# Kernel optimization log

Hardware: AMD Instinct MI355X
Metric: run time of the kernel (lower is better)

Reference implementation:

```python
import jax, jax.numpy as jnp
import numpy as np
from jax import lax

B, H, W, C = 8, 128, 128, 256


def setup_inputs() -> dict:
    key = jax.random.key(0)
    k1, k2 = jax.random.split(key)
    x = jax.random.normal(k1, (B, H, W, C), dtype=jnp.float32)
    # small-magnitude kernel so predicted offsets stay moderate (like trained init)
    kernel = jax.random.normal(k2, (3, 3, C, 2 * C), dtype=jnp.float32) * 0.01
    bias = jnp.zeros((2 * C,), dtype=jnp.float32)
    return {"x": x, "kernel": kernel, "bias": bias}


def _deform_sample(x, kernel, bias):
    b, h, w, c = x.shape
    # offset prediction conv: (b,h,w,c) -> (b,h,w,2c), SAME padding, stride 1
    offsets = lax.conv_general_dilated(
        x, kernel, window_strides=(1, 1), padding="SAME",
        dimension_numbers=("NHWC", "HWIO", "NHWC")) + bias
    # faithful reshape scaffolding from the original keras layer
    # (b,h,w,2c) -> (b,2c,h,w) -> (b*c, h, w, 2)
    offs = jnp.transpose(offsets, (0, 3, 1, 2)).reshape(b * c, h, w, 2)
    # (b,h,w,c) -> (b*c, h, w)
    xb = jnp.transpose(x, (0, 3, 1, 2)).reshape(b * c, h, w)

    n = h * w
    offs = offs.reshape(b * c, n, 2)
    grid = jnp.stack(jnp.meshgrid(jnp.arange(h), jnp.arange(w), indexing="ij"), axis=-1)
    grid = grid.reshape(n, 2).astype(x.dtype)  # (n,2) absolute (i,j)
    coords = offs + grid  # (b*c, n, 2)

    # original clips coord0 by w-1 and coord1 by h-1 (h==w assumed)
    c0 = jnp.clip(coords[..., 0], 0.0, jnp.float32(w - 1))
    c1 = jnp.clip(coords[..., 1], 0.0, jnp.float32(h - 1))
    coords = jnp.stack([c0, c1], axis=-1)

    lt = jnp.floor(coords).astype(jnp.int32)  # (b*c, n, 2)
    rb = jnp.ceil(coords).astype(jnp.int32)

    bidx = jnp.arange(b * c)[:, None]  # (b*c, 1) broadcast over n
    vals_lt = xb[bidx, lt[..., 0], lt[..., 1]]
    vals_rb = xb[bidx, rb[..., 0], rb[..., 1]]
    vals_lb = xb[bidx, lt[..., 0], rb[..., 1]]
    vals_rt = xb[bidx, rb[..., 0], lt[..., 1]]

    frac = coords - lt.astype(coords.dtype)  # (b*c, n, 2)
    vals_t = vals_lt + (vals_rt - vals_lt) * frac[..., 0]
    vals_b = vals_lb + (vals_rb - vals_lb) * frac[..., 0]
    mapped = vals_t + (vals_b - vals_t) * frac[..., 1]  # (b*c, n)

    # (b*c, h*w) -> (b, c, h, w) -> (b, h, w, c)
    return jnp.transpose(mapped.reshape(b, c, h, w), (0, 2, 3, 1))


def reference(x, kernel, bias):
    return _deform_sample(x, kernel, bias)
```

## Files before the change

kernel.cpp:

```cpp
#include <hip/hip_runtime.h>
#include <hip/hip_bf16.h>

#define BATCH 8
#define HH 128
#define WW 128
#define CC 256
#define OCC 512

typedef __bf16 bf16x8 __attribute__((ext_vector_type(8)));
typedef unsigned int u32x4 __attribute__((ext_vector_type(4)));
typedef float f32x4 __attribute__((ext_vector_type(4)));

#define WT_OFF   0
#define ZROW_OFF 2359296
#define XTB_OFF  2424832
#define XBF_OFF  69533696

__global__ void prep_weights(const float* __restrict__ k, __bf16* __restrict__ wt) {
    const int n   = blockIdx.x & 511;
    const int tap = blockIdx.x >> 9;
    const int ic  = threadIdx.x;
    const int oc  = ((n & 255) << 1) | (n >> 8);
    wt[((size_t)(tap * OCC + n)) * CC + ic] = (__bf16)k[((size_t)(tap * CC + ic)) * OCC + oc];
}

__global__ void zero_fill(float* __restrict__ z) {
    z[blockIdx.x * 256 + threadIdx.x] = 0.0f;
}

__global__ __launch_bounds__(256)
void prep_x(const float* __restrict__ x, __bf16* __restrict__ xbf, __bf16* __restrict__ xtb) {
    __shared__ float tile[64][65];
    const int pt = blockIdx.x & 3;
    const int mt = (blockIdx.x >> 2) & 255;
    const int b  = blockIdx.x >> 10;
    const int m0 = mt * 64, p0 = pt * 64;
    const int tl = threadIdx.x & 63, tr = threadIdx.x >> 6;

    const float* xb = x + (size_t)b * (HH * WW * CC);
    __bf16* xbfb = xbf + (size_t)b * (HH * WW * CC);
#pragma unroll
    for (int rr = 0; rr < 16; ++rr) {
        const int m = rr * 4 + tr;
        const float v = xb[(size_t)(m0 + m) * CC + p0 + tl];
        tile[m][tl] = v;
        xbfb[(size_t)(m0 + m) * CC + p0 + tl] = (__bf16)v;
    }
    __syncthreads();
    __bf16* xtbb = xtb + (size_t)b * (CC * HH * WW);
#pragma unroll
    for (int rr = 0; rr < 16; ++rr) {
        const int p = rr * 4 + tr;
        xtbb[(size_t)(p0 + p) * (HH * WW) + m0 + tl] = (__bf16)tile[tl][p];
    }
}

__device__ __forceinline__ void gload16(const void* g, void* l) {
    __builtin_amdgcn_global_load_lds(
        (const __attribute__((address_space(1))) void*)g,
        (__attribute__((address_space(3))) void*)l, 16, 0, 0);
}

__device__ __forceinline__ void stage_chunk(const __bf16* __restrict__ srcrow, int h,
                                            __bf16* ldsbuf, int wid, int lane) {
    const int sub = lane >> 4;
    const int icb = (lane & 15) * 16;
#pragma unroll
    for (int t = 0; t < 8; ++t) {
        const int col = (wid * 8 + t) * 4 + sub;
        const int srcoff = col * 512 + h * 256 + (icb ^ ((col & 7) << 4));
        gload16((const char*)srcrow + srcoff, (char*)ldsbuf + (wid * 8 + t) * 1024);
    }
}

__global__ __launch_bounds__(256, 2)
void conv_offset_sample(const __bf16* __restrict__ xbf, const __bf16* __restrict__ xtb,
                        const __bf16* __restrict__ zrow, const __bf16* __restrict__ wt,
                        const float* __restrict__ bias, float* __restrict__ out) {
    __shared__ __bf16 lds_a[2][16384];

    const int orig = blockIdx.x;
    const int bi = (orig & 7) * 512 + (orig >> 3);
    const int nc = bi & 3;
    const int cr = (bi >> 2) & 127;
    const int b  = bi >> 9;

    const int tid  = threadIdx.x;
    const int lane = tid & 63;
    const int wid  = tid >> 6;
    const int l15  = lane & 15;
    const int lg   = lane >> 4;

    f32x4 acc[2][8] = {};

    {
        const int rg = cr - 1;
        const __bf16* srcrow = ((unsigned)rg < 128u) ? xbf + ((size_t)(b * 128 + rg) << 15) : zrow;
        stage_chunk(srcrow, 0, lds_a[0], wid, lane);
    }
    __syncthreads();

    int cur = 0;
#pragma unroll 1
    for (int idx = 0; idx < 6; ++idx) {
        if (idx < 5) {
            const int n2 = idx + 1;
            const int rg = cr + (n2 >> 1) - 1;
            const __bf16* srcrow = ((unsigned)rg < 128u) ? xbf + ((size_t)(b * 128 + rg) << 15) : zrow;
            stage_chunk(srcrow, n2 & 1, lds_a[cur ^ 1], wid, lane);
        }
        const int r = idx >> 1;
        const int h = idx & 1;
        const __bf16* Ab = lds_a[cur];
        const int colb = wid * 32;

#pragma unroll
        for (int dx = 0; dx < 3; ++dx) {
            const __bf16* wtap = wt + ((size_t)((r * 3 + dx) * OCC + nc * 128)) * CC + h * 128;
#pragma unroll
            for (int kk = 0; kk < 4; ++kk) {
                bf16x8 a[2];
#pragma unroll
                for (int mi = 0; mi < 2; ++mi) {
                    const int ca = colb + mi * 16 + l15 + dx - 1;
                    const unsigned msk = ((unsigned)ca < 128u) ? 0xFFFFFFFFu : 0u;
                    const int ad = (((ca & 127) << 8) + ((kk * 32 + lg * 8) << 1)) ^ ((ca & 7) << 4);
                    u32x4 uv = *(const u32x4*)((const char*)Ab + ad);
                    uv &= msk;
                    a[mi] = __builtin_bit_cast(bf16x8, uv);
                }
#pragma unroll
                for (int ni = 0; ni < 8; ++ni) {
                    const bf16x8 bv = *(const bf16x8*)(wtap + (ni * 16 + l15) * CC + kk * 32 + lg * 8);
                    acc[0][ni] = __builtin_amdgcn_mfma_f32_16x16x32_bf16(a[0], bv, acc[0][ni], 0, 0, 0);
                    acc[1][ni] = __builtin_amdgcn_mfma_f32_16x16x32_bf16(a[1], bv, acc[1][ni], 0, 0, 0);
                }
            }
        }
        __syncthreads();
        cur ^= 1;
    }

    const int jbase = (cr & 1) << 6;
    const int par = nc >> 1;
    const int i2  = (cr >> 1) + (par << 6);
    const float fi2 = (float)i2;

#pragma unroll
    for (int ni = 0; ni < 8; ++ni) {
        const int p = ((nc & 1) << 7) + ni * 16 + l15;
        const float bv = bias[2 * p + par];
        const __bf16* plane = xtb + ((size_t)(b * 256 + p) << 14);
        float* op = out + (((size_t)(b * 128 + i2)) << 7) * 256 + p;

#pragma unroll
        for (int mi = 0; mi < 2; ++mi) {
#pragma unroll
            for (int s = 0; s < 2; ++s) {
                const int u  = wid * 16 + mi * 8 + lg * 2 + s;
                const int j2 = jbase + u;

                float c0 = acc[mi][ni][2 * s]     + bv + fi2;
                float c1 = acc[mi][ni][2 * s + 1] + bv + (float)j2;
                c0 = fminf(fmaxf(c0, 0.f), 127.f);
                c1 = fminf(fmaxf(c1, 0.f), 127.f);

                const int lt0 = (int)floorf(c0);
                const int rb0 = (int)ceilf(c0);
                const int lt1 = (int)floorf(c1);
                const int rb1 = (int)ceilf(c1);
                const float f0 = c0 - (float)lt0;
                const float f1 = c1 - (float)lt1;

                const float vlt = (float)plane[(lt0 << 7) + lt1];
                const float vrb = (float)plane[(rb0 << 7) + rb1];
                const float vlb = (float)plane[(lt0 << 7) + rb1];
                const float vrt = (float)plane[(rb0 << 7) + lt1];

                const float vt = vlt + (vrt - vlt) * f0;
                const float vb = vlb + (vrb - vlb) * f0;
                op[(size_t)j2 * 256] = vt + (vb - vt) * f1;
            }
        }
    }
}

extern "C" void kernel_launch(void* const* d_in, const int* in_sizes, int n_in,
                              void* d_out, int out_size, void* d_ws, size_t ws_size,
                              hipStream_t stream) {
    const float* x    = (const float*)d_in[0];
    const float* kern = (const float*)d_in[1];
    const float* bias = (const float*)d_in[2];
    float* out = (float*)d_out;

    __bf16* wt   = (__bf16*)((char*)d_ws + WT_OFF);
    __bf16* zrow = (__bf16*)((char*)d_ws + ZROW_OFF);
    __bf16* xtb  = (__bf16*)((char*)d_ws + XTB_OFF);
    __bf16* xbf  = (__bf16*)((char*)d_ws + XBF_OFF);

    prep_weights<<<4608, 256, 0, stream>>>(kern, wt);
    zero_fill<<<64, 256, 0, stream>>>((float*)zrow);
    prep_x<<<8192, 256, 0, stream>>>(x, xbf, xtb);
    conv_offset_sample<<<4096, 256, 0, stream>>>(xbf, xtb, zrow, wt, bias, out);
}
```

Before: 1.488 ms.

## Split fused conv+gather into a conv-coords pass and a separate gather kernel

When the workspace is large enough, the offset conv kernel now writes clipped sampling coordinates to a 256 MB fp32 buffer, and a second kernel does the bilinear gather with a layout that gives coalesced coordinate reads. The intent is to relieve the conv kernel of the scattered gather epilogue, which likely hurts occupancy and MFMA throughput, and to run the gather with better locality. The cost is an extra large write and read of intermediate data through HBM. The old fused path remains as a fallback when the workspace is too small.

```diff
diff --git a/kernel.cpp b/kernel.cpp
--- a/kernel.cpp
+++ b/kernel.cpp
@@ -15,6 +15,9 @@
 #define ZROW_OFF 2359296
 #define XTB_OFF  2424832
 #define XBF_OFF  69533696
+#define CV_OFF   136642560
+#define WS_NEED_SPLIT (CV_OFF + 268435456ull)
+#define WS_NEED_FUSED (XBF_OFF + 67108864ull)
 
 __global__ void prep_weights(const float* __restrict__ k, __bf16* __restrict__ wt) {
     const int n   = blockIdx.x & 511;
@@ -74,9 +77,9 @@
 }
 
 __global__ __launch_bounds__(256, 2)
-void conv_offset_sample(const __bf16* __restrict__ xbf, const __bf16* __restrict__ xtb,
-                        const __bf16* __restrict__ zrow, const __bf16* __restrict__ wt,
-                        const float* __restrict__ bias, float* __restrict__ out) {
+void conv_coords(const __bf16* __restrict__ xbf, const __bf16* __restrict__ zrow,
+                 const __bf16* __restrict__ wt, const float* __restrict__ bias,
+                 float* __restrict__ cv) {
     __shared__ __bf16 lds_a[2][16384];
 
     const int orig = blockIdx.x;
@@ -141,6 +144,146 @@
         cur ^= 1;
     }
 
+    const int par = nc >> 1;
+    const int i2  = (cr >> 1) + (par << 6);
+    const int jbase = (cr & 1) << 6;
+    const float fi2 = (float)i2;
+
+#pragma unroll
+    for (int ni = 0; ni < 8; ++ni) {
+        const int n = nc * 128 + ni * 16 + l15;
+        const float bv = bias[2 * (n & 255) + par];
+        float* cvp = cv + ((((size_t)b * 512 + n) * 128 + cr) << 7);
+#pragma unroll
+        for (int mi = 0; mi < 2; ++mi) {
+            const int j0 = wid * 32 + mi * 16 + lg * 4;
+            const int u0 = j0 >> 1;
+            f32x4 o;
+            o[0] = fminf(fmaxf(acc[mi][ni][0] + bv + fi2, 0.f), 127.f);
+            o[1] = fminf(fmaxf(acc[mi][ni][1] + bv + (float)(jbase + u0), 0.f), 127.f);
+            o[2] = fminf(fmaxf(acc[mi][ni][2] + bv + fi2, 0.f), 127.f);
+            o[3] = fminf(fmaxf(acc[mi][ni][3] + bv + (float)(jbase + u0 + 1), 0.f), 127.f);
+            *(f32x4*)(cvp + j0) = o;
+        }
+    }
+}
+
+__device__ __forceinline__ float bilerp(const __bf16* __restrict__ plane, float c0, float c1) {
+    const int lt0 = (int)floorf(c0);
+    const int rb0 = (int)ceilf(c0);
+    const int lt1 = (int)floorf(c1);
+    const int rb1 = (int)ceilf(c1);
+    const float f0 = c0 - (float)lt0;
+    const float f1 = c1 - (float)lt1;
+    const float vlt = (float)plane[(lt0 << 7) + lt1];
+    const float vrb = (float)plane[(rb0 << 7) + rb1];
+    const float vlb = (float)plane[(lt0 << 7) + rb1];
+    const float vrt = (float)plane[(rb0 << 7) + lt1];
+    const float vt = vlt + (vrt - vlt) * f0;
+    const float vb = vlb + (vrb - vlb) * f0;
+    return vt + (vb - vt) * f1;
+}
+
+__global__ __launch_bounds__(1024)
+void gather_out(const float* __restrict__ cv, const __bf16* __restrict__ xtb,
+                float* __restrict__ out) {
+    const int orig = blockIdx.x;
+    const int bi = (orig & 7) * 128 + (orig >> 3);
+    const int i2 = bi & 127;
+    const int b  = bi >> 7;
+
+    const int tid  = threadIdx.x;
+    const int lane = tid & 63;
+    const int w    = tid >> 6;
+
+    const int par  = i2 >> 6;
+    const int cr_a = (i2 & 63) << 1;
+    const int j2a  = ((lane >> 5) << 6) + ((lane & 31) << 1);
+
+    const float* cvb = cv + ((((size_t)b * 512) * 128 + cr_a) << 7);
+    float* ob = out + (((size_t)(b * 128 + i2)) << 7) * 256;
+
+#pragma unroll 1
+    for (int it = 0; it < 16; ++it) {
+        const int p = it * 16 + w;
+        const int n = p + (par << 8);
+        const f32x4 c = *(const f32x4*)(cvb + ((size_t)n << 14) + lane * 4);
+        const __bf16* plane = xtb + ((size_t)(b * 256 + p) << 14);
+        const float r0 = bilerp(plane, c[0], c[1]);
+        const float r1 = bilerp(plane, c[2], c[3]);
+        ob[(size_t)j2a * 256 + p] = r0;
+        ob[(size_t)(j2a + 1) * 256 + p] = r1;
+    }
+}
+
+__global__ __launch_bounds__(256, 2)
+void conv_offset_sample(const __bf16* __restrict__ xbf, const __bf16* __restrict__ xtb,
+                        const __bf16* __restrict__ zrow, const __bf16* __restrict__ wt,
+                        const float* __restrict__ bias, float* __restrict__ out) {
+    __shared__ __bf16 lds_a[2][16384];
+
+    const int orig = blockIdx.x;
+    const int bi = (orig & 7) * 512 + (orig >> 3);
+    const int nc = bi & 3;
+    const int cr = (bi >> 2) & 127;
+    const int b  = bi >> 9;
+
+    const int tid  = threadIdx.x;
+    const int lane = tid & 63;
+    const int wid  = tid >> 6;
+    const int l15  = lane & 15;
+    const int lg   = lane >> 4;
+
+    f32x4 acc[2][8] = {};
+
+    {
+        const int rg = cr - 1;
+        const __bf16* srcrow = ((unsigned)rg < 128u) ? xbf + ((size_t)(b * 128 + rg) << 15) : zrow;
+        stage_chunk(srcrow, 0, lds_a[0], wid, lane);
+    }
+    __syncthreads();
+
+    int cur = 0;
+#pragma unroll 1
+    for (int idx = 0; idx < 6; ++idx) {
+        if (idx < 5) {
+            const int n2 = idx + 1;
+            const int rg = cr + (n2 >> 1) - 1;
+            const __bf16* srcrow = ((unsigned)rg < 128u) ? xbf + ((size_t)(b * 128 + rg) << 15) : zrow;
+            stage_chunk(srcrow, n2 & 1, lds_a[cur ^ 1], wid, lane);
+        }
+        const int r = idx >> 1;
+        const int h = idx & 1;
+        const __bf16* Ab = lds_a[cur];
+        const int colb = wid * 32;
+
+#pragma unroll
+        for (int dx = 0; dx < 3; ++dx) {
+            const __bf16* wtap = wt + ((size_t)((r * 3 + dx) * OCC + nc * 128)) * CC + h * 128;
+#pragma unroll
+            for (int kk = 0; kk < 4; ++kk) {
+                bf16x8 a[2];
+#pragma unroll
+                for (int mi = 0; mi < 2; ++mi) {
+                    const int ca = colb + mi * 16 + l15 + dx - 1;
+                    const unsigned msk = ((unsigned)ca < 128u) ? 0xFFFFFFFFu : 0u;
+                    const int ad = (((ca & 127) << 8) + ((kk * 32 + lg * 8) << 1)) ^ ((ca & 7) << 4);
+                    u32x4 uv = *(const u32x4*)((const char*)Ab + ad);
+                    uv &= msk;
+                    a[mi] = __builtin_bit_cast(bf16x8, uv);
+                }
+#pragma unroll
+                for (int ni = 0; ni < 8; ++ni) {
+                    const bf16x8 bv = *(const bf16x8*)(wtap + (ni * 16 + l15) * CC + kk * 32 + lg * 8);
+                    acc[0][ni] = __builtin_amdgcn_mfma_f32_16x16x32_bf16(a[0], bv, acc[0][ni], 0, 0, 0);
+                    acc[1][ni] = __builtin_amdgcn_mfma_f32_16x16x32_bf16(a[1], bv, acc[1][ni], 0, 0, 0);
+                }
+            }
+        }
+        __syncthreads();
+        cur ^= 1;
+    }
+
     const int jbase = (cr & 1) << 6;
     const int par = nc >> 1;
     const int i2  = (cr >> 1) + (par << 6);
@@ -165,21 +308,8 @@
                 c0 = fminf(fmaxf(c0, 0.f), 127.f);
                 c1 = fminf(fmaxf(c1, 0.f), 127.f);
 
-                const int lt0 = (int)floorf(c0);
-                const int rb0 = (int)ceilf(c0);
-                const int lt1 = (int)floorf(c1);
-                const int rb1 = (int)ceilf(c1);
-                const float f0 = c0 - (float)lt0;
-                const float f1 = c1 - (float)lt1;
-
-                const float vlt = (float)plane[(lt0 << 7) + lt1];
-                const float vrb = (float)plane[(rb0 << 7) + rb1];
-                const float vlb = (float)plane[(lt0 << 7) + rb1];
-                const float vrt = (float)plane[(rb0 << 7) + lt1];
-
-                const float vt = vlt + (vrt - vlt) * f0;
-                const float vb = vlb + (vrb - vlb) * f0;
-                op[(size_t)j2 * 256] = vt + (vb - vt) * f1;
+                const float r = bilerp(plane, c0, c1);
+                op[(size_t)j2 * 256] = r;
             }
         }
     }
@@ -197,9 +327,16 @@
     __bf16* zrow = (__bf16*)((char*)d_ws + ZROW_OFF);
     __bf16* xtb  = (__bf16*)((char*)d_ws + XTB_OFF);
     __bf16* xbf  = (__bf16*)((char*)d_ws + XBF_OFF);
+    float*  cv   = (float*)((char*)d_ws + CV_OFF);
 
     prep_weights<<<4608, 256, 0, stream>>>(kern, wt);
     zero_fill<<<64, 256, 0, stream>>>((float*)zrow);
     prep_x<<<8192, 256, 0, stream>>>(x, xbf, xtb);
-    conv_offset_sample<<<4096, 256, 0, stream>>>(xbf, xtb, zrow, wt, bias, out);
-}
+
+    if (ws_size >= WS_NEED_SPLIT) {
+        conv_coords<<<4096, 256, 0, stream>>>(xbf, zrow, wt, bias, cv);
+        gather_out<<<1024, 1024, 0, stream>>>(cv, xtb, out);
+    } else {
+        conv_offset_sample<<<4096, 256, 0, stream>>>(xbf, xtb, zrow, wt, bias, out);
+    }
+}
```

After: 1.794 ms. 20.5% more time.
